# Kernel optimization log

Measured on AMD Instinct MI355X. Metric: run time of the kernel, lower is better.

Reference implementation:

```python
import jax, jax.numpy as jnp
import numpy as np

IMG = 512; P = 16; C = 3; DIM = 512; DEPTH = 2; HEADS = 8; HD = DIM // HEADS
MLP = 2048; W = 64; NCLS = 1000; B = 8
NPATCH = (IMG // P) ** 2          # 1024
N0 = NPATCH + 1                    # 1025 tokens incl CLS
PAD = (-N0) % (2 * W)              # pad to multiple of 2w (sliding_chunks)
N = N0 + PAD                       # 1152


def _ln(x, w, b):
    m = x.mean(-1, keepdims=True)
    v = jnp.mean((x - m) ** 2, -1, keepdims=True)
    return (x - m) * jax.lax.rsqrt(v + 1e-5) * w + b


def _heads(t):
    b, n, _ = t.shape
    return t.reshape(b, n, HEADS, HD).transpose(0, 2, 1, 3)  # b h n d


def _attn(x, mask, wq, bq, wk, bk, wv, bv, wqg, bqg, wkg, bkg, wvg, bvg):
    b, n, _ = x.shape
    sc = 1.0 / np.sqrt(HD)
    q = _heads(x @ wq + bq) * sc
    k = _heads(x @ wk + bk)
    v = _heads(x @ wv + bv)
    nc = n // W
    qc = q.reshape(b, HEADS, nc, W, HD)

    def chunk3(t):  # gather prev/self/next chunk of keys/values: b h nc 3W d
        tc = t.reshape(b, HEADS, nc, W, HD)
        z = jnp.zeros_like(tc[:, :, :1])
        prev = jnp.concatenate([z, tc[:, :, :-1]], 2)
        nxt = jnp.concatenate([tc[:, :, 1:], z], 2)
        return jnp.concatenate([prev, tc, nxt], 3)

    k3, v3 = chunk3(k), chunk3(v)
    band = jnp.einsum('bhcqd,bhckd->bhcqk', qc, k3)  # b h nc W 3W
    qi = jnp.arange(W)[:, None]
    kk = jnp.arange(3 * W)[None, :]
    rel_ok = jnp.abs(kk - W - qi) <= W               # exact +-w band
    kglob = jnp.arange(nc)[:, None, None] * W + (kk - W)[None]  # nc 1 3W
    in_rng = (kglob >= 0) & (kglob < n)
    kmask = mask[jnp.clip(kglob, 0, n - 1)]
    # keep only real local keys: exclude pad (0) and global (2, handled by gcol)
    keep = rel_ok[None] & in_rng & (kmask == 1.0)    # nc W 3W
    band = jnp.where(keep[None, None], band, -1e9)
    gcol = jnp.einsum('bhnd,bhd->bhn', q, k[:, :, 0])  # attend to global CLS key
    scores = jnp.concatenate([gcol[..., None], band.reshape(b, HEADS, n, 3 * W)], -1)
    a = jax.nn.softmax(scores, -1)                   # b h n (1+3W)
    out = jnp.einsum('bhcqk,bhckd->bhcqd', a[..., 1:].reshape(b, HEADS, nc, W, 3 * W), v3)
    out = out.reshape(b, HEADS, n, HD) + a[..., 0:1] * v[:, :, 0:1]
    # global CLS row attends to everything with its own projections
    qg0 = ((x[:, 0] @ wqg + bqg) * sc).reshape(b, HEADS, HD)
    kg = _heads(x @ wkg + bkg)
    vg = _heads(x @ wvg + bvg)
    gs = jnp.where(mask[None, None] > 0, jnp.einsum('bhd,bhnd->bhn', qg0, kg), -1e9)
    gout = jnp.einsum('bhn,bhnd->bhd', jax.nn.softmax(gs, -1), vg)
    out = out.at[:, :, 0].set(gout)
    return out.transpose(0, 2, 1, 3).reshape(b, n, DIM)


def setup_inputs():
    key = jax.random.key(0)
    ks = iter(jax.random.split(key, 20))

    def w(shape, s=0.02):
        return jax.random.normal(next(ks), shape, jnp.float32) * s

    return {
        'img': jax.random.normal(next(ks), (B, C, IMG, IMG), jnp.float32),
        'patch_w': w((P * P * C, DIM)), 'patch_b': jnp.zeros((DIM,), jnp.float32),
        'cls_tok': jax.random.uniform(next(ks), (1, 1, DIM), jnp.float32),
        'pos_emb': w((1, N0, DIM), 1.0),
        'ln1_w': jnp.ones((DEPTH, DIM), jnp.float32), 'ln1_b': jnp.zeros((DEPTH, DIM), jnp.float32),
        'wq': w((DEPTH, DIM, DIM)), 'bq': jnp.zeros((DEPTH, DIM), jnp.float32),
        'wk': w((DEPTH, DIM, DIM)), 'bk': jnp.zeros((DEPTH, DIM), jnp.float32),
        'wv': w((DEPTH, DIM, DIM)), 'bv': jnp.zeros((DEPTH, DIM), jnp.float32),
        'wqg': w((DEPTH, DIM, DIM)), 'bqg': jnp.zeros((DEPTH, DIM), jnp.float32),
        'wkg': w((DEPTH, DIM, DIM)), 'bkg': jnp.zeros((DEPTH, DIM), jnp.float32),
        'wvg': w((DEPTH, DIM, DIM)), 'bvg': jnp.zeros((DEPTH, DIM), jnp.float32),
        'ln2_w': jnp.ones((DEPTH, DIM), jnp.float32), 'ln2_b': jnp.zeros((DEPTH, DIM), jnp.float32),
        'w1': w((DEPTH, DIM, MLP)), 'b1': jnp.zeros((DEPTH, MLP), jnp.float32),
        'w2': w((DEPTH, MLP, DIM)), 'b2': jnp.zeros((DEPTH, DIM), jnp.float32),
        'head_ln_w': jnp.ones((DIM,), jnp.float32), 'head_ln_b': jnp.zeros((DIM,), jnp.float32),
        'head_w': w((DIM, NCLS)), 'head_b': jnp.zeros((NCLS,), jnp.float32),
    }


def reference(img, patch_w, patch_b, cls_tok, pos_emb, ln1_w, ln1_b, wq, bq, wk, bk,
              wv, bv, wqg, bqg, wkg, bkg, wvg, bvg, ln2_w, ln2_b, w1, b1, w2, b2,
              head_ln_w, head_ln_b, head_w, head_b):
    b = img.shape[0]
    hh = IMG // P
    # b c (h p1) (w p2) -> b (h w) (p1 p2 c)
    x = img.reshape(b, C, hh, P, hh, P).transpose(0, 2, 4, 3, 5, 1).reshape(b, hh * hh, P * P * C)
    x = x @ patch_w + patch_b
    x = jnp.concatenate([jnp.broadcast_to(cls_tok, (b, 1, DIM)), x], 1) + pos_emb
    x = jnp.pad(x, ((0, 0), (0, PAD), (0, 0)))
    mask = jnp.zeros((N,), jnp.float32).at[:N0].set(1.0).at[0].set(2.0)
    for i in range(DEPTH):
        x = x + _attn(_ln(x, ln1_w[i], ln1_b[i]), mask,
                      wq[i], bq[i], wk[i], bk[i], wv[i], bv[i],
                      wqg[i], bqg[i], wkg[i], bkg[i], wvg[i], bvg[i])
        h = jax.nn.gelu(_ln(x, ln2_w[i], ln2_b[i]) @ w1[i] + b1[i], approximate=False)
        x = x + h @ w2[i] + b2[i]
    cls = x[:, 0]  # pool='cls'
    return _ln(cls, head_ln_w, head_ln_b) @ head_w + head_b
```

## Files before the change

kernel.cpp:

```cpp
#include <hip/hip_runtime.h>
#include <hip/hip_bf16.h>
#include <math.h>

typedef __hip_bfloat16 bf16;
typedef float f32x4 __attribute__((ext_vector_type(4)));
typedef short s16x8 __attribute__((ext_vector_type(8)));
typedef short s16x4 __attribute__((ext_vector_type(4)));
typedef unsigned int u32;
typedef unsigned long long u64;

#define NB 8
#define NROW 1025
#define MTOT (NB*NROW)
#define DIMD 512
#define NHEAD 8
#define HD 64
#define MLPD 2048
#define QKVN 2560
#define JSTR 1032
#define GTILE 8

__device__ __forceinline__ float b2f(short u) {
    return __builtin_bit_cast(float, (u32)(unsigned short)u << 16);
}
__device__ __forceinline__ unsigned short f2bfbits(float f) {
    __hip_bfloat16 h = __float2bfloat16(f);
    return __builtin_bit_cast(unsigned short, h);
}
__device__ __forceinline__ void g2lds16(const bf16* g, bf16* l) {
    __builtin_amdgcn_global_load_lds((const __attribute__((address_space(1))) u32*)g,
                                     (__attribute__((address_space(3))) u32*)l, 16, 0, 0);
}

__global__ __launch_bounds__(256) void transpose_cvt_L(
    const float* __restrict__ src, bf16* __restrict__ dst, int K, int N, float scale)
{
    __shared__ float t[32][33];
    const int z = blockIdx.z;
    const float* s = src + (size_t)z * K * N;
    bf16* d = dst + (size_t)z * N * K;
    const int n0 = blockIdx.x * 32, k0 = blockIdx.y * 32;
    const int tx = threadIdx.x, ty = threadIdx.y;
#pragma unroll
    for (int i = 0; i < 32; i += 8)
        t[ty + i][tx] = s[(long)(k0 + ty + i) * N + n0 + tx];
    __syncthreads();
#pragma unroll
    for (int i = 0; i < 32; i += 8)
        d[(long)(n0 + ty + i) * K + k0 + tx] = __float2bfloat16(t[tx][ty + i] * scale);
}

__global__ __launch_bounds__(256) void qkvw_t(
    const float* __restrict__ wq, const float* __restrict__ wk, const float* __restrict__ wv,
    const float* __restrict__ wkg, const float* __restrict__ wvg, bf16* __restrict__ qkvT)
{
    __shared__ float t[32][33];
    const int z = blockIdx.z, L = z / 5, s = z % 5;
    const float* srcs[5] = {wq, wk, wv, wkg, wvg};
    const float* src = srcs[s] + (size_t)L * DIMD * DIMD;
    bf16* dst = qkvT + ((size_t)L * QKVN + s * DIMD) * DIMD;
    const float scale = (s == 0) ? 0.125f : 1.f;
    const int n0 = blockIdx.x * 32, k0 = blockIdx.y * 32;
    const int tx = threadIdx.x, ty = threadIdx.y;
#pragma unroll
    for (int i = 0; i < 32; i += 8)
        t[ty + i][tx] = src[(long)(k0 + ty + i) * DIMD + n0 + tx];
    __syncthreads();
#pragma unroll
    for (int i = 0; i < 32; i += 8)
        dst[(long)(n0 + ty + i) * DIMD + k0 + tx] = __float2bfloat16(t[tx][ty + i] * scale);
}

__global__ __launch_bounds__(256) void build_bias(
    const float* __restrict__ bq, const float* __restrict__ bk, const float* __restrict__ bv,
    const float* __restrict__ bkg, const float* __restrict__ bvg, float* __restrict__ outb)
{
    int idx = blockIdx.x * 256 + threadIdx.x;
    if (idx >= 2 * QKVN) return;
    int L = idx / QKVN, c = idx % QKVN;
    int sec = c >> 9, d = c & 511;
    const float* src = (sec == 0) ? bq : (sec == 1) ? bk : (sec == 2) ? bv : (sec == 3) ? bkg : bvg;
    float v = src[L * DIMD + d];
    if (sec == 0) v *= 0.125f;
    outb[idx] = v;
}

__global__ __launch_bounds__(256) void im2col(
    const float* __restrict__ img, bf16* __restrict__ A)
{
    const int idx = blockIdx.x * 256 + threadIdx.x;
    const int pp = idx & 7;
    const int pw = (idx >> 3) & 31;
    const int py = (idx >> 8) & 15;
    const int ph = (idx >> 12) & 31;
    const int b  = idx >> 17;
    const int hh = ph * 16 + py;
    const int w  = pw * 16 + pp * 2;
    const float2 c0 = *(const float2*)(img + (((long)(b * 3 + 0) * 512 + hh) * 512 + w));
    const float2 c1 = *(const float2*)(img + (((long)(b * 3 + 1) * 512 + hh) * 512 + w));
    const float2 c2 = *(const float2*)(img + (((long)(b * 3 + 2) * 512 + hh) * 512 + w));
    const long row = (long)b * 1024 + ph * 32 + pw;
    u32* dst = (u32*)(A + row * 768 + py * 48 + pp * 6);
    dst[0] = (u32)f2bfbits(c0.x) | ((u32)f2bfbits(c1.x) << 16);
    dst[1] = (u32)f2bfbits(c2.x) | ((u32)f2bfbits(c0.y) << 16);
    dst[2] = (u32)f2bfbits(c1.y) | ((u32)f2bfbits(c2.y) << 16);
}

__global__ __launch_bounds__(256) void cls_row(
    const float* __restrict__ cls, const float* __restrict__ pos, float* __restrict__ x)
{
    const int idx = blockIdx.x * 256 + threadIdx.x;
    const int b = idx >> 9, d = idx & 511;
    x[(long)b * NROW * DIMD + d] = cls[d] + pos[d];
}

__global__ __launch_bounds__(256) void ln_fwd(
    const float* __restrict__ x, const float* __restrict__ w,
    const float* __restrict__ bb, bf16* __restrict__ y, int Mrows)
{
    const int row = blockIdx.x * 4 + (threadIdx.x >> 6);
    if (row >= Mrows) return;
    const int lane = threadIdx.x & 63;
    const float* xr = x + (long)row * DIMD + lane * 8;
    float4 a = *(const float4*)xr;
    float4 b4 = *(const float4*)(xr + 4);
    float s  = a.x + a.y + a.z + a.w + b4.x + b4.y + b4.z + b4.w;
    float sq = a.x*a.x + a.y*a.y + a.z*a.z + a.w*a.w + b4.x*b4.x + b4.y*b4.y + b4.z*b4.z + b4.w*b4.w;
#pragma unroll
    for (int o = 32; o; o >>= 1) { s += __shfl_xor(s, o); sq += __shfl_xor(sq, o); }
    float mean = s * (1.f / 512.f);
    float rstd = rsqrtf(sq * (1.f / 512.f) - mean * mean + 1e-5f);
    bf16* yr = y + (long)row * DIMD + lane * 8;
    const float* wp = w + lane * 8;
    const float* bp = bb + lane * 8;
    float vals[8] = {a.x, a.y, a.z, a.w, b4.x, b4.y, b4.z, b4.w};
#pragma unroll
    for (int u = 0; u < 8; ++u)
        yr[u] = __float2bfloat16((vals[u] - mean) * rstd * wp[u] + bp[u]);
}

template<int EPI>
__global__ __launch_bounds__(256) void gemm128(
    const bf16* __restrict__ A, const bf16* __restrict__ Bt,
    const float* __restrict__ bias,
    float* __restrict__ Cf, bf16* __restrict__ Cb,
    int M, int N, int K, const float* __restrict__ posp, bf16* __restrict__ vTout)
{
    __shared__ bf16 aL[2][128 * 64];
    __shared__ bf16 bL[2][128 * 64];
    const int tid = threadIdx.x, lane = tid & 63, w = tid >> 6;
    const int m0 = blockIdx.y * 128, n0 = blockIdx.x * 128;
    const int wm = w >> 1, wn = w & 1;
    f32x4 acc[4][4] = {};
    const int nk = K >> 6;
    const int srow = lane >> 3;
    const int scol = ((lane & 7) ^ srow) * 8;

#define STAGE(buf, kt) do {                                                        \
        _Pragma("unroll")                                                          \
        for (int i = 0; i < 4; ++i) {                                              \
            const int rb = i * 32 + w * 8;                                         \
            long ar = m0 + rb + srow; if (ar >= M) ar = M - 1;                     \
            g2lds16(A  + ar * (long)K + (long)(kt) * 64 + scol, &aL[buf][rb * 64]);\
            g2lds16(Bt + (long)(n0 + rb + srow) * K + (long)(kt) * 64 + scol,      \
                    &bL[buf][rb * 64]);                                            \
        } } while (0)

    STAGE(0, 0);
    __syncthreads();
    int cur = 0;
    const int fr = lane & 15;
    const int lc0 = lane >> 4;
    const int px = lane & 7;
    const int arow_b = (wm * 64 + fr) << 7;
    const int brow_b = (wn * 64 + fr) << 7;
    for (int kt = 0; kt < nk; ++kt) {
        if (kt + 1 < nk) STAGE(cur ^ 1, kt + 1);
        const char* aP = (const char*)&aL[cur][0];
        const char* bP = (const char*)&bL[cur][0];
#pragma unroll
        for (int ksub = 0; ksub < 2; ++ksub) {
            const int cb = ((ksub * 4 + lc0) ^ px) << 4;
            s16x8 af[4], bf_[4];
#pragma unroll
            for (int mi = 0; mi < 4; ++mi) af[mi]  = *(const s16x8*)(aP + arow_b + mi * 2048 + cb);
#pragma unroll
            for (int ni = 0; ni < 4; ++ni) bf_[ni] = *(const s16x8*)(bP + brow_b + ni * 2048 + cb);
#pragma unroll
            for (int mi = 0; mi < 4; ++mi)
#pragma unroll
                for (int ni = 0; ni < 4; ++ni)
                    acc[mi][ni] = __builtin_amdgcn_mfma_f32_16x16x32_bf16(af[mi], bf_[ni], acc[mi][ni], 0, 0, 0);
        }
        __syncthreads();
        cur ^= 1;
    }
#undef STAGE
    const int lr = (lane >> 4) * 4, lc = lane & 15;
    bf16* cT = &aL[0][0];
#pragma unroll
    for (int mi = 0; mi < 4; ++mi) {
        const int row0 = wm * 64 + mi * 16 + lr;
        const int gr0 = m0 + row0;
#pragma unroll
        for (int ni = 0; ni < 4; ++ni) {
            const int colL = wn * 64 + ni * 16 + lc;
            const int gc = n0 + colL;
            const float bv = bias[gc];
            if (EPI == 1 || EPI == 2) {
                unsigned short pk[4];
#pragma unroll
                for (int j = 0; j < 4; ++j) {
                    float v = acc[mi][ni][j] + bv;
                    if (EPI == 2) v = 0.5f * v * (1.f + erff(v * 0.70710678118f));
                    const bf16 hv = __float2bfloat16(v);
                    cT[(row0 + j) * 128 + colL] = hv;
                    pk[j] = (gr0 + j < M) ? __builtin_bit_cast(unsigned short, hv)
                                          : (unsigned short)0;
                }
                if (EPI == 1 && gc >= 1024 && gc < 1536) {
                    const int d = gc - 1024;
                    const int bb2 = gr0 / NROW, jj = gr0 - bb2 * NROW;
                    if (jj <= 1021 && gr0 + 3 < M) {
                        u64 pack =  (u64)pk[0] | ((u64)pk[1] << 16)
                                 | ((u64)pk[2] << 32) | ((u64)pk[3] << 48);
                        *(u64*)&vTout[((long)bb2 * 512 + d) * JSTR + jj] = pack;
                    } else {
#pragma unroll
                        for (int j = 0; j < 4; ++j) {
                            const int gr = gr0 + j;
                            if (gr < M) {
                                const int b3 = gr / NROW, j3 = gr - b3 * NROW;
                                vTout[((long)b3 * 512 + d) * JSTR + j3] =
                                    __builtin_bit_cast(bf16, pk[j]);
                            }
                        }
                    }
                }
            } else {
#pragma unroll
                for (int j = 0; j < 4; ++j) {
                    const int gr = gr0 + j;
                    if (gr < M) {
                        float v = acc[mi][ni][j] + bv;
                        if (EPI == 0) Cf[(long)gr * N + gc] = v;
                        else if (EPI == 3) Cf[(long)gr * N + gc] += v;
                        else {
                            const int bb2 = gr >> 10, pidx = gr & 1023;
                            Cf[((long)bb2 * NROW + 1 + pidx) * DIMD + gc]
                                = v + posp[(long)(pidx + 1) * DIMD + gc];
                        }
                    }
                }
            }
        }
    }
    if (EPI == 1 || EPI == 2) {
        __syncthreads();
        const int row = tid >> 1, half = tid & 1;
        const int gr = m0 + row;
        if (gr < M) {
            bf16* dst = Cb + (long)gr * N + n0 + half * 64;
            const bf16* srcRow = cT + row * 128 + half * 64;
#pragma unroll
            for (int k = 0; k < 8; ++k) {
                const int kk = (k + row) & 7;
                *(s16x8*)(dst + kk * 8) = *(const s16x8*)(srcRow + kk * 8);
            }
        }
    }
}

__global__ __launch_bounds__(256) void gemm_n64(
    const bf16* __restrict__ A, const bf16* __restrict__ Bt,
    const float* __restrict__ bias, float* __restrict__ Cf,
    int M, int N, int K)
{
    __shared__ bf16 aL[2][128 * 64];
    __shared__ bf16 bL[2][64 * 64];
    const int tid = threadIdx.x, lane = tid & 63, w = tid >> 6;
    const int m0 = blockIdx.y * 128, n0 = blockIdx.x * 64;
    f32x4 acc[2][4] = {};
    const int nk = K >> 6;
    const int srow = lane >> 3;
    const int scol = ((lane & 7) ^ srow) * 8;

#define STAGEN(buf, kt) do {                                                       \
        _Pragma("unroll")                                                          \
        for (int i = 0; i < 4; ++i) {                                              \
            const int rb = i * 32 + w * 8;                                         \
            long ar = m0 + rb + srow; if (ar >= M) ar = M - 1;                     \
            g2lds16(A + ar * (long)K + (long)(kt) * 64 + scol, &aL[buf][rb * 64]); \
        }                                                                          \
        _Pragma("unroll")                                                          \
        for (int i = 0; i < 2; ++i) {                                              \
            const int rb = i * 32 + w * 8;                                         \
            g2lds16(Bt + (long)(n0 + rb + srow) * K + (long)(kt) * 64 + scol,      \
                    &bL[buf][rb * 64]);                                            \
        } } while (0)

    STAGEN(0, 0);
    __syncthreads();
    int cur = 0;
    const int fr = lane & 15;
    const int lc0 = lane >> 4;
    const int px = lane & 7;
    const int arow_b = (w * 32 + fr) << 7;
    const int brow_b = fr << 7;
    for (int kt = 0; kt < nk; ++kt) {
        if (kt + 1 < nk) STAGEN(cur ^ 1, kt + 1);
        const char* aP = (const char*)&aL[cur][0];
        const char* bP = (const char*)&bL[cur][0];
#pragma unroll
        for (int ksub = 0; ksub < 2; ++ksub) {
            const int cb = ((ksub * 4 + lc0) ^ px) << 4;
            s16x8 af[2], bf_[4];
#pragma unroll
            for (int mi = 0; mi < 2; ++mi) af[mi]  = *(const s16x8*)(aP + arow_b + mi * 2048 + cb);
#pragma unroll
            for (int ni = 0; ni < 4; ++ni) bf_[ni] = *(const s16x8*)(bP + brow_b + ni * 2048 + cb);
#pragma unroll
            for (int mi = 0; mi < 2; ++mi)
#pragma unroll
                for (int ni = 0; ni < 4; ++ni)
                    acc[mi][ni] = __builtin_amdgcn_mfma_f32_16x16x32_bf16(af[mi], bf_[ni], acc[mi][ni], 0, 0, 0);
        }
        __syncthreads();
        cur ^= 1;
    }
#undef STAGEN
    const int lr = (lane >> 4) * 4, lc = lane & 15;
#pragma unroll
    for (int mi = 0; mi < 2; ++mi) {
        const int gr0 = m0 + w * 32 + mi * 16 + lr;
#pragma unroll
        for (int ni = 0; ni < 4; ++ni) {
            const int gc = n0 + ni * 16 + lc;
            const float bv = bias[gc];
#pragma unroll
            for (int j = 0; j < 4; ++j) {
                const int gr = gr0 + j;
                if (gr < M) Cf[(long)gr * N + gc] += acc[mi][ni][j] + bv;
            }
        }
    }
}

__global__ __launch_bounds__(256) void qg_proj(
    const bf16* __restrict__ ybf, const float* __restrict__ wqg,
    const float* __restrict__ bqg, float* __restrict__ qg_all)
{
    __shared__ float y0[512];
    const int b = blockIdx.x, tid = threadIdx.x;
    const long rowb = (long)b * NROW;
    for (int d = tid; d < 512; d += 256) y0[d] = __bfloat162float(ybf[rowb * DIMD + d]);
    __syncthreads();
    const int c = blockIdx.y * 256 + tid;
    float a = 0.f;
#pragma unroll 8
    for (int kk = 0; kk < 512; ++kk) a += y0[kk] * wqg[(long)kk * DIMD + c];
    qg_all[b * DIMD + c] = (a + bqg[c]) * 0.125f;
}

__global__ __launch_bounds__(256) void band_glob_attn(
    const bf16* __restrict__ qkv, const bf16* __restrict__ vT,
    const float* __restrict__ qg_all, float* __restrict__ gpart, float* __restrict__ x)
{
    __shared__ bf16 KlPl[193 * 72];
    __shared__ bf16 Vt[64 * 192];
    const int c = blockIdx.x, h = blockIdx.y, b = blockIdx.z;
    const int tid = threadIdx.x, lane = tid & 63, w = tid >> 6;
    const long rowb = (long)b * NROW;
    const int hoff = h * HD;

    if (c >= 16) {
        const int t = c - 16;
        const int j0 = t * 129;
        const int len = (1025 - j0) < 129 ? (1025 - j0) : 129;
        float* gsh  = (float*)KlPl;
        float* S    = gsh;
        float* qgs  = gsh + 160;
        float* redx = gsh + 224;
        const int dd = tid & 63, part = tid >> 6;
        if (tid < 64) qgs[tid] = qg_all[b * DIMD + hoff + tid];
        __syncthreads();
        if (tid < len) {
            const bf16* kr = qkv + (rowb + j0 + tid) * QKVN + 1536 + hoff;
            float s = 0.f;
#pragma unroll
            for (int c8 = 0; c8 < 8; ++c8) {
                s16x8 kv = *(const s16x8*)(kr + c8 * 8);
#pragma unroll
                for (int e = 0; e < 8; ++e) s += qgs[c8 * 8 + e] * b2f(kv[e]);
            }
            S[tid] = s;
        }
        __syncthreads();
        float lm = -1e30f;
        for (int j = tid; j < len; j += 256) lm = fmaxf(lm, S[j]);
        redx[tid] = lm; __syncthreads();
        for (int st = 128; st; st >>= 1) { if (tid < st) redx[tid] = fmaxf(redx[tid], redx[tid + st]); __syncthreads(); }
        const float mt = redx[0]; __syncthreads();
        float ls = 0.f;
        for (int j = tid; j < len; j += 256) { float e = __expf(S[j] - mt); S[j] = e; ls += e; }
        redx[tid] = ls; __syncthreads();
        for (int st = 128; st; st >>= 1) { if (tid < st) redx[tid] += redx[tid + st]; __syncthreads(); }
        const float tsum = redx[0];
        __syncthreads();
        float acc = 0.f;
#pragma unroll 4
        for (int j = part; j < len; j += 4)
            acc += S[j] * __bfloat162float(qkv[(rowb + j0 + j) * QKVN + 2048 + hoff + dd]);
        redx[tid] = acc;
        __syncthreads();
        if (part == 0) {
            float* gp = gpart + ((size_t)((b * NHEAD + h) * GTILE + t)) * 66;
            gp[2 + dd] = redx[dd] + redx[64 + dd] + redx[128 + dd] + redx[192 + dd];
            if (dd == 0) { gp[0] = mt; gp[1] = tsum; }
        }
        return;
    }

    const int qi0 = 1 + c * 64, jbase = qi0 - 64;
    bf16* Kl = KlPl;

    for (int task = tid; task < 193 * 8; task += 256) {
        const int d8 = task & 7, r = task >> 3;
        int j = (r < 192) ? (jbase + r) : 0;
        j = j < 0 ? 0 : (j > 1024 ? 1024 : j);
        s16x8 val = *(const s16x8*)(qkv + (rowb + j) * QKVN + 512 + hoff + d8 * 8);
        *(s16x8*)(Kl + r * 72 + d8 * 8) = val;
    }
    for (int task = tid; task < 64 * 24; task += 256) {
        const int kc = task % 24, d = task / 24;
        int j0 = jbase + kc * 8;
        j0 = j0 < 0 ? 0 : (j0 > 1017 ? 1017 : j0);
        s16x8 v = *(const s16x8*)(vT + ((long)(b * 512 + hoff + d)) * JSTR + j0);
        const int bo = (d * 384 + kc * 16) ^ ((d & 7) << 4);
        *(s16x8*)((char*)Vt + bo) = v;
    }

    const int q = lane & 15, g = lane >> 4;
    const int qg = w * 16 + q;
    s16x8 qf0, qf1;
    {
        const bf16* qp = qkv + (rowb + qi0 + qg) * QKVN + hoff + g * 8;
        qf0 = *(const s16x8*)qp;
        qf1 = *(const s16x8*)(qp + 32);
    }
    __syncthreads();

    f32x4 sc[13] = {};
#pragma unroll
    for (int nt = 0; nt < 13; ++nt) {
        const bf16* kp = Kl + (nt * 16 + q) * 72 + g * 8;
        s16x8 k0 = *(const s16x8*)kp;
        s16x8 k1 = *(const s16x8*)(kp + 32);
        sc[nt] = __builtin_amdgcn_mfma_f32_16x16x32_bf16(k0, qf0, sc[nt], 0, 0, 0);
        sc[nt] = __builtin_amdgcn_mfma_f32_16x16x32_bf16(k1, qf1, sc[nt], 0, 0, 0);
    }

    const int lo_ = (qg > 1 - jbase) ? qg : 1 - jbase;
    const int hi_ = (qg + 128 < 1024 - jbase) ? qg + 128 : 1024 - jbase;
    float m = -1e30f;
#pragma unroll
    for (int nt = 0; nt < 12; ++nt)
#pragma unroll
        for (int j = 0; j < 4; ++j) {
            const int slot = nt * 16 + g * 4 + j;
            float s = (slot >= lo_ && slot <= hi_) ? sc[nt][j] : -1e9f;
            sc[nt][j] = s;
            m = fmaxf(m, s);
        }
#pragma unroll
    for (int j = 0; j < 4; ++j) {
        float s = (g == 0 && j == 0) ? sc[12][j] : -1e9f;
        sc[12][j] = s;
        m = fmaxf(m, s);
    }
    m = fmaxf(m, __shfl_xor(m, 16));
    m = fmaxf(m, __shfl_xor(m, 32));
    float sum = 0.f;
#pragma unroll
    for (int nt = 0; nt < 13; ++nt)
#pragma unroll
        for (int j = 0; j < 4; ++j) {
            float p = __expf(sc[nt][j] - m);
            sc[nt][j] = p;
            sum += p;
        }
    sum += __shfl_xor(sum, 16);
    sum += __shfl_xor(sum, 32);
    const float inv = 1.f / sum;
    const float a0 = __shfl(sc[12][0], q);

    __syncthreads();

    char* plw = (char*)KlPl + w * 6144;
#pragma unroll
    for (int nt = 0; nt < 12; ++nt) {
        u32 lo2 = (u32)f2bfbits(sc[nt][0]) | ((u32)f2bfbits(sc[nt][1]) << 16);
        u32 hi2 = (u32)f2bfbits(sc[nt][2]) | ((u32)f2bfbits(sc[nt][3]) << 16);
        const int bo = (q * 384 + (nt * 16 + g * 4) * 2) ^ ((q & 7) << 4);
        *(uint2*)(plw + bo) = make_uint2(lo2, hi2);
    }
    __syncthreads();

    f32x4 ac[4] = {};
#pragma unroll
    for (int ks = 0; ks < 6; ++ks) {
        const int pbo = (q * 384 + (ks * 32 + g * 8) * 2) ^ ((q & 7) << 4);
        s16x8 pf = *(const s16x8*)(plw + pbo);
#pragma unroll
        for (int mt = 0; mt < 4; ++mt) {
            const int d = mt * 16 + q;
            const int vbo = ((d * 192 + ks * 32 + g * 8) * 2) ^ ((d & 7) << 4);
            s16x8 vf = *(const s16x8*)((char*)Vt + vbo);
            ac[mt] = __builtin_amdgcn_mfma_f32_16x16x32_bf16(vf, pf, ac[mt], 0, 0, 0);
        }
    }

    const bf16* v0p = qkv + rowb * QKVN + 1024 + hoff;
    float* xr = x + (rowb + qi0 + qg) * DIMD + hoff;
#pragma unroll
    for (int mt = 0; mt < 4; ++mt) {
        const int d0 = mt * 16 + g * 4;
        const s16x4 vv = *(const s16x4*)(v0p + d0);
        float4 prev = *(float4*)(xr + d0);
        prev.x += (ac[mt][0] + a0 * b2f(vv[0])) * inv;
        prev.y += (ac[mt][1] + a0 * b2f(vv[1])) * inv;
        prev.z += (ac[mt][2] + a0 * b2f(vv[2])) * inv;
        prev.w += (ac[mt][3] + a0 * b2f(vv[3])) * inv;
        *(float4*)(xr + d0) = prev;
    }
}

__global__ __launch_bounds__(64) void glob_merge(
    const float* __restrict__ gp, float* __restrict__ x)
{
    const int hb = blockIdx.x;
    const int b = hb >> 3, h = hb & 7;
    const int dd = threadIdx.x;
    const float* base = gp + (size_t)hb * GTILE * 66;
    float m = -1e30f;
#pragma unroll
    for (int t = 0; t < GTILE; ++t) m = fmaxf(m, base[t * 66]);
    float sum = 0.f, acc = 0.f;
#pragma unroll
    for (int t = 0; t < GTILE; ++t) {
        const float wgt = __expf(base[t * 66] - m);
        sum += wgt * base[t * 66 + 1];
        acc += wgt * base[t * 66 + 2 + dd];
    }
    x[(long)b * NROW * DIMD + h * HD + dd] += acc / sum;
}

__global__ __launch_bounds__(512) void lncls(
    const float* __restrict__ x, const float* __restrict__ lw,
    const float* __restrict__ lb, float* __restrict__ out)
{
    const int b = threadIdx.x >> 6, lane = threadIdx.x & 63;
    const int d0 = lane * 8;
    const float* xr = x + (long)b * NROW * DIMD + d0;
    float4 a = *(const float4*)xr;
    float4 b4 = *(const float4*)(xr + 4);
    float s  = a.x + a.y + a.z + a.w + b4.x + b4.y + b4.z + b4.w;
    float sq = a.x*a.x + a.y*a.y + a.z*a.z + a.w*a.w + b4.x*b4.x + b4.y*b4.y + b4.z*b4.z + b4.w*b4.w;
#pragma unroll
    for (int o = 32; o; o >>= 1) { s += __shfl_xor(s, o); sq += __shfl_xor(sq, o); }
    const float mean = s * (1.f / 512.f);
    const float rstd = rsqrtf(sq * (1.f / 512.f) - mean * mean + 1e-5f);
    float vals[8] = {a.x, a.y, a.z, a.w, b4.x, b4.y, b4.z, b4.w};
#pragma unroll
    for (int u = 0; u < 8; ++u)
        out[b * DIMD + d0 + u] = (vals[u] - mean) * rstd * lw[d0 + u] + lb[d0 + u];
}

__global__ __launch_bounds__(128) void head_gemv(
    const float* __restrict__ lnc, const float* __restrict__ hw,
    const float* __restrict__ hb, float* __restrict__ out)
{
    const int idx = blockIdx.x * 128 + threadIdx.x;
    if (idx >= NB * 1000) return;
    const int b = idx / 1000, cc = idx - b * 1000;
    const float* lr = lnc + b * DIMD;
    float a = hb[cc];
#pragma unroll 8
    for (int kk = 0; kk < 512; ++kk) a += lr[kk] * hw[(long)kk * 1000 + cc];
    out[idx] = a;
}

extern "C" void kernel_launch(void* const* d_in, const int* in_sizes, int n_in,
                              void* d_out, int out_size, void* d_ws, size_t ws_size,
                              hipStream_t stream)
{
    const float* img     = (const float*)d_in[0];
    const float* patch_w = (const float*)d_in[1];
    const float* patch_b = (const float*)d_in[2];
    const float* cls_tok = (const float*)d_in[3];
    const float* pos_emb = (const float*)d_in[4];
    const float* ln1_w   = (const float*)d_in[5];
    const float* ln1_b   = (const float*)d_in[6];
    const float* wq  = (const float*)d_in[7];
    const float* bq  = (const float*)d_in[8];
    const float* wk  = (const float*)d_in[9];
    const float* bk  = (const float*)d_in[10];
    const float* wv  = (const float*)d_in[11];
    const float* bv  = (const float*)d_in[12];
    const float* wqg = (const float*)d_in[13];
    const float* bqg = (const float*)d_in[14];
    const float* wkg = (const float*)d_in[15];
    const float* bkg = (const float*)d_in[16];
    const float* wvg = (const float*)d_in[17];
    const float* bvg = (const float*)d_in[18];
    const float* ln2_w = (const float*)d_in[19];
    const float* ln2_b = (const float*)d_in[20];
    const float* w1 = (const float*)d_in[21];
    const float* b1 = (const float*)d_in[22];
    const float* w2 = (const float*)d_in[23];
    const float* b2 = (const float*)d_in[24];
    const float* hlw = (const float*)d_in[25];
    const float* hlb = (const float*)d_in[26];
    const float* hw  = (const float*)d_in[27];
    const float* hb  = (const float*)d_in[28];

    char* wsb = (char*)d_ws;
    size_t o = 0;
    auto carve = [&](size_t n) { size_t r = o; o += (n + 255) & ~(size_t)255; return r; };
    float* x    = (float*)(wsb + carve((size_t)MTOT * DIMD * 4));
    bf16*  ybf  = (bf16*) (wsb + carve((size_t)MTOT * DIMD * 2));
    bf16*  qkv  = (bf16*) (wsb + carve((size_t)MTOT * QKVN * 2));
    bf16*  hbuf = (bf16*) (wsb + carve((size_t)MTOT * MLPD * 2));
    bf16*  vT   = (bf16*) (wsb + carve((size_t)NB * 512 * JSTR * 2));
    bf16*  acol = (bf16*) (wsb + carve((size_t)8192 * 768 * 2));
    bf16*  pwt  = (bf16*) (wsb + carve((size_t)512 * 768 * 2));
    bf16*  qkvT = (bf16*) (wsb + carve((size_t)2 * QKVN * DIMD * 2));
    bf16*  w1t  = (bf16*) (wsb + carve((size_t)2 * MLPD * DIMD * 2));
    bf16*  w2t  = (bf16*) (wsb + carve((size_t)2 * DIMD * MLPD * 2));
    float* catb = (float*)(wsb + carve((size_t)2 * QKVN * 4));
    float* qg_all = (float*)(wsb + carve((size_t)NB * DIMD * 4));
    float* gpart  = (float*)(wsb + carve((size_t)NB * NHEAD * GTILE * 66 * 4));
    float* lnc  = (float*)(wsb + carve((size_t)NB * DIMD * 4));
    (void)ws_size; (void)in_sizes; (void)n_in; (void)out_size;

    dim3 tb(32, 8);
    transpose_cvt_L<<<dim3(16, 24, 1), tb, 0, stream>>>(patch_w, pwt, 768, 512, 1.f);
    qkvw_t<<<dim3(16, 16, 10), tb, 0, stream>>>(wq, wk, wv, wkg, wvg, qkvT);
    transpose_cvt_L<<<dim3(64, 16, 2), tb, 0, stream>>>(w1, w1t, DIMD, MLPD, 1.f);
    transpose_cvt_L<<<dim3(16, 64, 2), tb, 0, stream>>>(w2, w2t, MLPD, DIMD, 1.f);
    build_bias<<<20, 256, 0, stream>>>(bq, bk, bv, bkg, bvg, catb);

    im2col<<<4096, 256, 0, stream>>>(img, acol);
    gemm128<4><<<dim3(4, 64), 256, 0, stream>>>(
        acol, pwt, patch_b, x, nullptr, 8192, 512, 768, pos_emb, nullptr);
    cls_row<<<16, 256, 0, stream>>>(cls_tok, pos_emb, x);

    for (int L = 0; L < 2; ++L) {
        ln_fwd<<<2050, 256, 0, stream>>>(x, ln1_w + L * DIMD, ln1_b + L * DIMD, ybf, MTOT);
        gemm128<1><<<dim3(QKVN/128, 65), 256, 0, stream>>>(
            ybf, qkvT + (size_t)L * QKVN * DIMD, catb + L * QKVN, nullptr, qkv,
            MTOT, QKVN, DIMD, nullptr, vT);
        qg_proj<<<dim3(NB, 2), 256, 0, stream>>>(
            ybf, wqg + (size_t)L * DIMD * DIMD, bqg + L * DIMD, qg_all);
        band_glob_attn<<<dim3(16 + GTILE, NHEAD, NB), 256, 0, stream>>>(
            qkv, vT, qg_all, gpart, x);
        glob_merge<<<NB * NHEAD, 64, 0, stream>>>(gpart, x);
        ln_fwd<<<2050, 256, 0, stream>>>(x, ln2_w + L * DIMD, ln2_b + L * DIMD, ybf, MTOT);
        gemm128<2><<<dim3(MLPD/128, 65), 256, 0, stream>>>(
            ybf, w1t + (size_t)L * MLPD * DIMD, b1 + L * MLPD, nullptr, hbuf,
            MTOT, MLPD, DIMD, nullptr, nullptr);
        gemm_n64<<<dim3(DIMD/64, 65), 256, 0, stream>>>(
            hbuf, w2t + (size_t)L * DIMD * MLPD, b2 + L * DIMD, x, MTOT, DIMD, MLPD);
    }
    lncls<<<1, 512, 0, stream>>>(x, hlw, hlb, lnc);
    head_gemv<<<63, 128, 0, stream>>>(lnc, hw, hb, (float*)d_out);
}
```

Baseline: 520.1 us.

## Fuse global query projection into attention kernel; write GELU output directly

```diff
diff --git a/kernel.cpp b/kernel.cpp
--- a/kernel.cpp
+++ b/kernel.cpp
@@ -207,18 +207,16 @@
             const int colL = wn * 64 + ni * 16 + lc;
             const int gc = n0 + colL;
             const float bv = bias[gc];
-            if (EPI == 1 || EPI == 2) {
+            if (EPI == 1) {
                 unsigned short pk[4];
 #pragma unroll
                 for (int j = 0; j < 4; ++j) {
-                    float v = acc[mi][ni][j] + bv;
-                    if (EPI == 2) v = 0.5f * v * (1.f + erff(v * 0.70710678118f));
-                    const bf16 hv = __float2bfloat16(v);
+                    const bf16 hv = __float2bfloat16(acc[mi][ni][j] + bv);
                     cT[(row0 + j) * 128 + colL] = hv;
                     pk[j] = (gr0 + j < M) ? __builtin_bit_cast(unsigned short, hv)
                                           : (unsigned short)0;
                 }
-                if (EPI == 1 && gc >= 1024 && gc < 1536) {
+                if (gc >= 1024 && gc < 1536) {
                     const int d = gc - 1024;
                     const int bb2 = gr0 / NROW, jj = gr0 - bb2 * NROW;
                     if (jj <= 1021 && gr0 + 3 < M) {
@@ -244,8 +242,12 @@
                     if (gr < M) {
                         float v = acc[mi][ni][j] + bv;
                         if (EPI == 0) Cf[(long)gr * N + gc] = v;
-                        else if (EPI == 3) Cf[(long)gr * N + gc] += v;
-                        else {
+                        else if (EPI == 2) {
+                            float g = 0.5f * v * (1.f + erff(v * 0.70710678118f));
+                            Cb[(long)gr * N + gc] = __float2bfloat16(g);
+                        } else if (EPI == 3) {
+                            Cf[(long)gr * N + gc] += v;
+                        } else {
                             const int bb2 = gr >> 10, pidx = gr & 1023;
                             Cf[((long)bb2 * NROW + 1 + pidx) * DIMD + gc]
                                 = v + posp[(long)(pidx + 1) * DIMD + gc];
@@ -255,7 +257,7 @@
             }
         }
     }
-    if (EPI == 1 || EPI == 2) {
+    if (EPI == 1) {
         __syncthreads();
         const int row = tid >> 1, half = tid & 1;
         const int gr = m0 + row;
@@ -346,25 +348,10 @@
     }
 }
 
-__global__ __launch_bounds__(256) void qg_proj(
-    const bf16* __restrict__ ybf, const float* __restrict__ wqg,
-    const float* __restrict__ bqg, float* __restrict__ qg_all)
-{
-    __shared__ float y0[512];
-    const int b = blockIdx.x, tid = threadIdx.x;
-    const long rowb = (long)b * NROW;
-    for (int d = tid; d < 512; d += 256) y0[d] = __bfloat162float(ybf[rowb * DIMD + d]);
-    __syncthreads();
-    const int c = blockIdx.y * 256 + tid;
-    float a = 0.f;
-#pragma unroll 8
-    for (int kk = 0; kk < 512; ++kk) a += y0[kk] * wqg[(long)kk * DIMD + c];
-    qg_all[b * DIMD + c] = (a + bqg[c]) * 0.125f;
-}
-
 __global__ __launch_bounds__(256) void band_glob_attn(
     const bf16* __restrict__ qkv, const bf16* __restrict__ vT,
-    const float* __restrict__ qg_all, float* __restrict__ gpart, float* __restrict__ x)
+    const bf16* __restrict__ ybf, const float* __restrict__ wqg,
+    const float* __restrict__ bqg, float* __restrict__ gpart, float* __restrict__ x)
 {
     __shared__ bf16 KlPl[193 * 72];
     __shared__ bf16 Vt[64 * 192];
@@ -378,11 +365,23 @@
         const int j0 = t * 129;
         const int len = (1025 - j0) < 129 ? (1025 - j0) : 129;
         float* gsh  = (float*)KlPl;
-        float* S    = gsh;
-        float* qgs  = gsh + 160;
-        float* redx = gsh + 224;
+        float* y0   = gsh;
+        float* S    = gsh + 512;
+        float* qgs  = gsh + 672;
+        float* redx = gsh + 736;
         const int dd = tid & 63, part = tid >> 6;
-        if (tid < 64) qgs[tid] = qg_all[b * DIMD + hoff + tid];
+        for (int d = tid; d < 512; d += 256) y0[d] = __bfloat162float(ybf[rowb * DIMD + d]);
+        __syncthreads();
+        {
+            float a = 0.f;
+            for (int kk = part; kk < 512; kk += 4)
+                a += y0[kk] * wqg[(long)kk * DIMD + hoff + dd];
+            redx[tid] = a;
+        }
+        __syncthreads();
+        if (part == 0)
+            qgs[dd] = (redx[dd] + redx[64 + dd] + redx[128 + dd] + redx[192 + dd]
+                       + bqg[hoff + dd]) * 0.125f;
         __syncthreads();
         if (tid < len) {
             const bf16* kr = qkv + (rowb + j0 + tid) * QKVN + 1536 + hoff;
@@ -638,7 +637,6 @@
     bf16*  w1t  = (bf16*) (wsb + carve((size_t)2 * MLPD * DIMD * 2));
     bf16*  w2t  = (bf16*) (wsb + carve((size_t)2 * DIMD * MLPD * 2));
     float* catb = (float*)(wsb + carve((size_t)2 * QKVN * 4));
-    float* qg_all = (float*)(wsb + carve((size_t)NB * DIMD * 4));
     float* gpart  = (float*)(wsb + carve((size_t)NB * NHEAD * GTILE * 66 * 4));
     float* lnc  = (float*)(wsb + carve((size_t)NB * DIMD * 4));
     (void)ws_size; (void)in_sizes; (void)n_in; (void)out_size;
@@ -660,10 +658,8 @@
         gemm128<1><<<dim3(QKVN/128, 65), 256, 0, stream>>>(
             ybf, qkvT + (size_t)L * QKVN * DIMD, catb + L * QKVN, nullptr, qkv,
             MTOT, QKVN, DIMD, nullptr, vT);
-        qg_proj<<<dim3(NB, 2), 256, 0, stream>>>(
-            ybf, wqg + (size_t)L * DIMD * DIMD, bqg + L * DIMD, qg_all);
         band_glob_attn<<<dim3(16 + GTILE, NHEAD, NB), 256, 0, stream>>>(
-            qkv, vT, qg_all, gpart, x);
+            qkv, vT, ybf, wqg + (size_t)L * DIMD * DIMD, bqg + L * DIMD, gpart, x);
         glob_merge<<<NB * NHEAD, 64, 0, stream>>>(gpart, x);
         ln_fwd<<<2050, 256, 0, stream>>>(x, ln2_w + L * DIMD, ln2_b + L * DIMD, ybf, MTOT);
         gemm128<2><<<dim3(MLPD/128, 65), 256, 0, stream>>>(
```

Result: slower. 545.3 us (+4.8%).
